# Kernel optimization log

Measured on AMD Instinct MI355X. Metric: run time of the kernel, lower is better.

## Reference

```python
import jax, jax.numpy as jnp
import numpy as np

HID = 100

def _make_params(key):
    dims = [(2, HID), (HID, HID), (HID, HID), (HID, HID), (HID, 2)]
    params = {}
    for i, (fan_in, fan_out) in enumerate(dims):
        k1, k2, key = jax.random.split(key, 3)
        bound = 1.0 / np.sqrt(fan_in)
        params[f"W{i+1}"] = jax.random.uniform(k1, (fan_out, fan_in), jnp.float32, -bound, bound)
        params[f"b{i+1}"] = jax.random.uniform(k2, (fan_out,), jnp.float32, -bound, bound)
    return params

def setup_inputs() -> dict:
    key = jax.random.key(0)
    kx, kt, kp = jax.random.split(key, 3)
    N = 262144
    inp = {
        "x": jax.random.normal(kx, (N, 1), jnp.float32),
        "t": jax.random.uniform(kt, (N, 1), jnp.float32),
    }
    inp.update(_make_params(kp))
    return inp

def reference(x, t, W1, b1, W2, b2, W3, b3, W4, b4, W5, b5):
    hidden = [(W1, b1), (W2, b2), (W3, b3), (W4, b4)]

    def u(xs, ts):  # scalar xs, ts -> [2] = (u_r, u_i)
        h = jnp.stack([xs, ts])
        for W, b in hidden:
            h = jnp.tanh(W @ h + b)
        return W5 @ h + b5

    u_t = jax.jacfwd(u, argnums=1)          # [2]: (u_t_r, u_t_i)
    u_x = jax.jacfwd(u, argnums=0)          # [2]
    u_xx = jax.jacfwd(u_x, argnums=0)       # [2]: (u_xx_r, u_xx_i)

    def per_point(xs, ts):
        return u(xs, ts), u_t(xs, ts), u_xx(xs, ts)

    U, Ut, Uxx = jax.vmap(per_point)(x[:, 0], t[:, 0])  # each [N, 2]

    u_r, u_i = U[:, 0:1], U[:, 1:2]
    u_t_r, u_t_i = Ut[:, 0:1], Ut[:, 1:2]
    u_xx_r, u_xx_i = Uxx[:, 0:1], Uxx[:, 1:2]

    mag2 = u_r * u_r + u_i * u_i
    f_r = -u_t_i + 0.5 * u_xx_r + mag2 * u_r
    f_i = u_t_r + 0.5 * u_xx_i + mag2 * u_i
    return f_r, f_i
```

## Files before the change

### kernel.cpp

```cpp
#include <hip/hip_runtime.h>


using half8 = __attribute__((ext_vector_type(8))) _Float16;
using half4 = __attribute__((ext_vector_type(4))) _Float16;
using f32x4 = __attribute__((ext_vector_type(4))) float;

#define LW      44800
#define ZOFF    134400
#define STGOFF  134416
#define STGW    2304
#define PLANEB  1152
#define NWAVES  12
#define SMEM_BYTES 162064

union U8 { uint4 u; half8 h; };
union U4 { uint2 u; half4 h; };

static __device__ __forceinline__ float fast_tanh(float z) {
    float e = __expf(2.0f * z);
    return 1.0f - 2.0f * __builtin_amdgcn_rcpf(e + 1.0f);
}

static __device__ __forceinline__ void split2(float v, _Float16& h0, _Float16& h1) {
    h0 = (_Float16)v;
    h1 = (_Float16)((v - (float)h0) * 512.0f);
}

__global__ void prep_w(const float* __restrict__ W2, const float* __restrict__ W3,
                       const float* __restrict__ W4, unsigned short* __restrict__ ws) {
    int bid = blockIdx.x;
    int l = bid / 28, rem = bid % 28, kt = rem / 7, jt = rem % 7;
    const float* W = (l == 0) ? W2 : (l == 1) ? W3 : W4;
    int lane = threadIdx.x;
    int c = lane & 15, q = lane >> 4;
    int j = 16 * jt + c;
    if (kt < 3) {
        for (int s = 0; s < 2; ++s)
            for (int i = 0; i < 8; ++i) {
                int k = 32 * kt + 8 * q + i;
                float w = (j < 100) ? W[j * 100 + k] : 0.0f;
                _Float16 h0 = (_Float16)w;
                _Float16 val = (s == 0) ? h0 : (_Float16)((w - (float)h0) * 512.0f);
                ws[(l*LW + kt*14336 + jt*2048 + s*1024 + lane*16 + i*2) >> 1] =
                    __builtin_bit_cast(unsigned short, val);
            }
    } else if (lane < 16) {
        for (int s = 0; s < 2; ++s)
            for (int i = 0; i < 4; ++i) {
                int k = 96 + i;
                float w = (j < 100) ? W[j * 100 + k] : 0.0f;
                _Float16 h0 = (_Float16)w;
                _Float16 val = (s == 0) ? h0 : (_Float16)((w - (float)h0) * 512.0f);
                ws[(l*LW + 43008 + jt*256 + s*128 + lane*8 + i*2) >> 1] =
                    __builtin_bit_cast(unsigned short, val);
            }
    }
}

__global__ void __launch_bounds__(768) pinn_mfma(
    const float* __restrict__ x,  const float* __restrict__ t,
    const float* __restrict__ W1, const float* __restrict__ b1,
    const float* __restrict__ b2, const float* __restrict__ b3,
    const float* __restrict__ b4,
    const float* __restrict__ W5, const float* __restrict__ b5,
    const char* __restrict__ ws, float* __restrict__ out,
    int N, int nchunks)
{
    extern __shared__ char smem[];
    const int tid  = threadIdx.x;
    const int w    = tid >> 6;
    const int lane = tid & 63;
    const int c15  = lane & 15;
    const int q    = lane >> 4;

    for (int it = 0; it < 11; ++it) {
        int idx = tid + it * 768;
        if (idx < 8400) ((uint4*)smem)[idx] = ((const uint4*)ws)[idx];
    }
    if (tid < 4) *(unsigned*)(smem + ZOFF + tid * 4) = 0u;
    __syncthreads();

    char* stg = smem + STGOFF + w * STGW;

    half8 a0[3], a1[3];
    half4 a0t,   a1t;
    f32x4 c0[7], c1[7];

    for (int chunk = blockIdx.x; chunk < nchunks; chunk += gridDim.x) {
        const int colbase = chunk * 192 + w * 16;

        {
            int col = colbase + c15;
            int pt = col >> 2, ch = col & 3;
            int ptc = (pt < N) ? pt : (N - 1);
            float xv = x[ptc], tv = t[ptc];
            #pragma unroll
            for (int kt = 0; kt < 3; ++kt) {
                half8 v0, v1;
                #pragma unroll
                for (int i = 0; i < 8; ++i) {
                    int j = 32 * kt + 8 * q + i;
                    float w0 = W1[2*j], w1 = W1[2*j+1], bb = b1[j];
                    float p = fmaf(w0, xv, fmaf(w1, tv, bb));
                    float a = fast_tanh(p);
                    float s = 1.0f - a * a;
                    float v = (ch == 0) ? a : (ch == 1) ? s * w1
                             : (ch == 2) ? s * w0 : -2.0f * a * s * w0 * w0;
                    _Float16 h0, h1; split2(v, h0, h1);
                    v0[i] = h0; v1[i] = h1;
                }
                a0[kt] = v0; a1[kt] = v1;
            }
            half4 t0 = {0, 0, 0, 0}, t1 = {0, 0, 0, 0};
            if (q == 0) {
                #pragma unroll
                for (int i = 0; i < 4; ++i) {
                    int j = 96 + i;
                    float w0 = W1[2*j], w1 = W1[2*j+1], bb = b1[j];
                    float p = fmaf(w0, xv, fmaf(w1, tv, bb));
                    float a = fast_tanh(p);
                    float s = 1.0f - a * a;
                    float v = (ch == 0) ? a : (ch == 1) ? s * w1
                             : (ch == 2) ? s * w0 : -2.0f * a * s * w0 * w0;
                    _Float16 h0, h1; split2(v, h0, h1);
                    t0[i] = h0; t1[i] = h1;
                }
            }
            a0t = t0; a1t = t1;
        }

        for (int l = 0; l < 3; ++l) {
            const char* WL = smem + l * LW;
            const float* BL = (l == 0) ? b2 : (l == 1) ? b3 : b4;

            #pragma unroll
            for (int jt = 0; jt < 7; ++jt) {
                c0[jt] = (f32x4){0.f, 0.f, 0.f, 0.f};
                c1[jt] = (f32x4){0.f, 0.f, 0.f, 0.f};
            }

            #pragma unroll
            for (int kt = 0; kt < 3; ++kt)
                #pragma unroll
                for (int jt = 0; jt < 7; ++jt) {
                    U8 b0u, b1u;
                    b0u.u = *(const uint4*)(WL + kt*14336 + jt*2048 + lane*16);
                    b1u.u = *(const uint4*)(WL + kt*14336 + jt*2048 + 1024 + lane*16);
                    c0[jt] = __builtin_amdgcn_mfma_f32_16x16x32_f16(a0[kt], b0u.h, c0[jt], 0, 0, 0);
                    c1[jt] = __builtin_amdgcn_mfma_f32_16x16x32_f16(a0[kt], b1u.h, c1[jt], 0, 0, 0);
                    c1[jt] = __builtin_amdgcn_mfma_f32_16x16x32_f16(a1[kt], b0u.h, c1[jt], 0, 0, 0);
                }
            #pragma unroll
            for (int jt = 0; jt < 7; ++jt) {
                int toff  = (lane < 16) ? (l*LW + 43008 + jt*256 + lane*8) : ZOFF;
                int toff1 = (lane < 16) ? (toff + 128) : ZOFF;
                U4 b0u, b1u;
                b0u.u = *(const uint2*)(smem + toff);
                b1u.u = *(const uint2*)(smem + toff1);
                c0[jt] = __builtin_amdgcn_mfma_f32_16x16x16f16(a0t, b0u.h, c0[jt], 0, 0, 0);
                c1[jt] = __builtin_amdgcn_mfma_f32_16x16x16f16(a0t, b1u.h, c1[jt], 0, 0, 0);
                c1[jt] = __builtin_amdgcn_mfma_f32_16x16x16f16(a1t, b0u.h, c1[jt], 0, 0, 0);
            }

            if (l < 2) {
                #pragma unroll
                for (int kc = 0; kc < 4; ++kc) {
                    int njt = (kc < 3) ? 2 : 1;
                    #pragma unroll
                    for (int jj = 0; jj < 2; ++jj) {
                        if (jj >= njt) continue;
                        int jt = 2 * kc + jj;
                        int kk = 16 * jj + c15;
                        int j  = 16 * jt + c15;
                        float bj = BL[(j < 100) ? j : 99];
                        float z0 = c0[jt][0] + c1[jt][0] * (1.0f/512.0f) + bj;
                        float z1 = c0[jt][1] + c1[jt][1] * (1.0f/512.0f);
                        float z2 = c0[jt][2] + c1[jt][2] * (1.0f/512.0f);
                        float z3 = c0[jt][3] + c1[jt][3] * (1.0f/512.0f);
                        float a = fast_tanh(z0);
                        float s = 1.0f - a * a;
                        float v[4];
                        v[0] = a; v[1] = s * z1; v[2] = s * z2;
                        v[3] = fmaf(-2.0f * a * s * z2, z2, s * z3);
                        #pragma unroll
                        for (int r = 0; r < 4; ++r) {
                            _Float16 h0, h1; split2(v[r], h0, h1);
                            _Float16* bp = (_Float16*)(stg) + (4 * q + r) * 36 + kk;
                            bp[0]   = h0;
                            bp[576] = h1;
                        }
                    }
                    if (kc < 3) {
                        const char* rb = stg + c15 * 72 + 16 * q;
                        U8 u;
                        uint2 L, H;
                        L = *(const uint2*)(rb);              H = *(const uint2*)(rb + 8);
                        u.u = (uint4){L.x, L.y, H.x, H.y};    a0[kc] = u.h;
                        L = *(const uint2*)(rb + PLANEB);     H = *(const uint2*)(rb + PLANEB + 8);
                        u.u = (uint4){L.x, L.y, H.x, H.y};    a1[kc] = u.h;
                    } else {
                        U4 u;
                        if (q == 0) {
                            const char* rb = stg + c15 * 72;
                            u.u = *(const uint2*)(rb);            a0t = u.h;
                            u.u = *(const uint2*)(rb + PLANEB);   a1t = u.h;
                        } else {
                            a0t = (half4){0,0,0,0}; a1t = (half4){0,0,0,0};
                        }
                    }
                }
            } else {
                float p00 = 0.f, p01 = 0.f, p03 = 0.f;
                float p10 = 0.f, p11 = 0.f, p13 = 0.f;
                #pragma unroll
                for (int jt = 0; jt < 7; ++jt) {
                    int j = 16 * jt + c15;
                    int j2 = (j < 100) ? j : 99;
                    float m = (j < 100) ? 1.0f : 0.0f;
                    float bj = BL[j2];
                    float w50 = W5[j2] * m, w51 = W5[100 + j2] * m;
                    float z0 = c0[jt][0] + c1[jt][0] * (1.0f/512.0f) + bj;
                    float z1 = c0[jt][1] + c1[jt][1] * (1.0f/512.0f);
                    float z2 = c0[jt][2] + c1[jt][2] * (1.0f/512.0f);
                    float z3 = c0[jt][3] + c1[jt][3] * (1.0f/512.0f);
                    float a = fast_tanh(z0);
                    float s = 1.0f - a * a;
                    float v0 = a, v1 = s * z1;
                    float v3 = fmaf(-2.0f * a * s * z2, z2, s * z3);
                    p00 = fmaf(w50, v0, p00);
                    p01 = fmaf(w50, v1, p01);
                    p03 = fmaf(w50, v3, p03);
                    p10 = fmaf(w51, v0, p10);
                    p11 = fmaf(w51, v1, p11);
                    p13 = fmaf(w51, v3, p13);
                }
                #pragma unroll
                for (int m = 1; m <= 8; m <<= 1) {
                    p00 += __shfl_xor(p00, m, 64);
                    p01 += __shfl_xor(p01, m, 64);
                    p03 += __shfl_xor(p03, m, 64);
                    p10 += __shfl_xor(p10, m, 64);
                    p11 += __shfl_xor(p11, m, 64);
                    p13 += __shfl_xor(p13, m, 64);
                }
                int pt = chunk * 48 + w * 4 + q;
                if (c15 == 0 && pt < N) {
                    float ur = p00 + b5[0], ui = p10 + b5[1];
                    float mag2 = ur * ur + ui * ui;
                    float fr = fmaf(mag2, ur, fmaf(0.5f, p03, -p11));
                    float fi = fmaf(mag2, ui, fmaf(0.5f, p13,  p01));
                    out[pt]     = fr;
                    out[N + pt] = fi;
                }
            }
        }
    }
}

extern "C" void kernel_launch(void* const* d_in, const int* in_sizes, int n_in,
                              void* d_out, int out_size, void* d_ws, size_t ws_size,
                              hipStream_t stream) {
    const float* x  = (const float*)d_in[0];
    const float* t  = (const float*)d_in[1];
    const float* W1 = (const float*)d_in[2];
    const float* b1 = (const float*)d_in[3];
    const float* W2 = (const float*)d_in[4];
    const float* b2 = (const float*)d_in[5];
    const float* W3 = (const float*)d_in[6];
    const float* b3 = (const float*)d_in[7];
    const float* W4 = (const float*)d_in[8];
    const float* b4 = (const float*)d_in[9];
    const float* W5 = (const float*)d_in[10];
    const float* b5 = (const float*)d_in[11];
    float* out = (float*)d_out;
    const int N = in_sizes[0];
    const int nchunks = (N + 47) / 48;

    (void)hipFuncSetAttribute((const void*)pinn_mfma,
                              hipFuncAttributeMaxDynamicSharedMemorySize, SMEM_BYTES);

    prep_w<<<84, 64, 0, stream>>>(W2, W3, W4, (unsigned short*)d_ws);
    pinn_mfma<<<256, 768, SMEM_BYTES, stream>>>(x, t, W1, b1, b2, b3, b4, W5, b5,
                                                (const char*)d_ws, out, N, nchunks);
}
```

Baseline: 437.6 us.

## Read MFMA weight fragments from global memory instead of staging in LDS

Drops the per-block copy of all three hidden-layer weight matrices (about 134 KB) into shared memory and has each wave load its B fragments straight from the global workspace, which should hit in L1/L2. Blocks shrink from 12 waves to 4 waves with only a small static LDS staging area, and launch bounds now allow several blocks per CU. The grid grows to 2048 blocks, each taking a contiguous range of chunks. This removes the large LDS fill and the occupancy cap of one block per CU, at the cost of far more global/L1 traffic in the inner MFMA loop.

```diff
diff --git a/kernel.cpp b/kernel.cpp
--- a/kernel.cpp
+++ b/kernel.cpp
@@ -6,12 +6,10 @@
 using f32x4 = __attribute__((ext_vector_type(4))) float;
 
 #define LW      44800
-#define ZOFF    134400
-#define STGOFF  134416
+#define WZOFF   134400
 #define STGW    2304
 #define PLANEB  1152
-#define NWAVES  12
-#define SMEM_BYTES 162064
+#define SMEM_BYTES 9216
 
 union U8 { uint4 u; half8 h; };
 union U4 { uint2 u; half4 h; };
@@ -29,9 +27,13 @@
 __global__ void prep_w(const float* __restrict__ W2, const float* __restrict__ W3,
                        const float* __restrict__ W4, unsigned short* __restrict__ ws) {
     int bid = blockIdx.x;
+    int lane = threadIdx.x;
+    if (bid == 84) {
+        if (lane < 8) ws[(WZOFF >> 1) + lane] = 0;
+        return;
+    }
     int l = bid / 28, rem = bid % 28, kt = rem / 7, jt = rem % 7;
     const float* W = (l == 0) ? W2 : (l == 1) ? W3 : W4;
-    int lane = threadIdx.x;
     int c = lane & 15, q = lane >> 4;
     int j = 16 * jt + c;
     if (kt < 3) {
@@ -57,37 +59,33 @@
     }
 }
 
-__global__ void __launch_bounds__(768) pinn_mfma(
+__global__ void __launch_bounds__(256, 4) pinn_mfma(
     const float* __restrict__ x,  const float* __restrict__ t,
     const float* __restrict__ W1, const float* __restrict__ b1,
     const float* __restrict__ b2, const float* __restrict__ b3,
     const float* __restrict__ b4,
     const float* __restrict__ W5, const float* __restrict__ b5,
     const char* __restrict__ ws, float* __restrict__ out,
-    int N, int nchunks)
+    int N, int nchunks, int cpb)
 {
-    extern __shared__ char smem[];
+    __shared__ char smem[SMEM_BYTES];
     const int tid  = threadIdx.x;
     const int w    = tid >> 6;
     const int lane = tid & 63;
     const int c15  = lane & 15;
     const int q    = lane >> 4;
 
-    for (int it = 0; it < 11; ++it) {
-        int idx = tid + it * 768;
-        if (idx < 8400) ((uint4*)smem)[idx] = ((const uint4*)ws)[idx];
-    }
-    if (tid < 4) *(unsigned*)(smem + ZOFF + tid * 4) = 0u;
-    __syncthreads();
-
-    char* stg = smem + STGOFF + w * STGW;
+    char* stg = smem + w * STGW;
 
     half8 a0[3], a1[3];
     half4 a0t,   a1t;
     f32x4 c0[7], c1[7];
 
-    for (int chunk = blockIdx.x; chunk < nchunks; chunk += gridDim.x) {
-        const int colbase = chunk * 192 + w * 16;
+    const int cbeg = blockIdx.x * cpb;
+    const int cend = (cbeg + cpb < nchunks) ? (cbeg + cpb) : nchunks;
+
+    for (int chunk = cbeg; chunk < cend; ++chunk) {
+        const int colbase = chunk * 64 + w * 16;
 
         {
             int col = colbase + c15;
@@ -130,7 +128,7 @@
         }
 
         for (int l = 0; l < 3; ++l) {
-            const char* WL = smem + l * LW;
+            const char* WL = ws + l * LW;
             const float* BL = (l == 0) ? b2 : (l == 1) ? b3 : b4;
 
             #pragma unroll
@@ -152,11 +150,11 @@
                 }
             #pragma unroll
             for (int jt = 0; jt < 7; ++jt) {
-                int toff  = (lane < 16) ? (l*LW + 43008 + jt*256 + lane*8) : ZOFF;
-                int toff1 = (lane < 16) ? (toff + 128) : ZOFF;
+                int toff  = (lane < 16) ? (l*LW + 43008 + jt*256 + lane*8) : WZOFF;
+                int toff1 = (lane < 16) ? (toff + 128) : WZOFF;
                 U4 b0u, b1u;
-                b0u.u = *(const uint2*)(smem + toff);
-                b1u.u = *(const uint2*)(smem + toff1);
+                b0u.u = *(const uint2*)(ws + toff);
+                b1u.u = *(const uint2*)(ws + toff1);
                 c0[jt] = __builtin_amdgcn_mfma_f32_16x16x16f16(a0t, b0u.h, c0[jt], 0, 0, 0);
                 c1[jt] = __builtin_amdgcn_mfma_f32_16x16x16f16(a0t, b1u.h, c1[jt], 0, 0, 0);
                 c1[jt] = __builtin_amdgcn_mfma_f32_16x16x16f16(a1t, b0u.h, c1[jt], 0, 0, 0);
@@ -243,7 +241,7 @@
                     p11 += __shfl_xor(p11, m, 64);
                     p13 += __shfl_xor(p13, m, 64);
                 }
-                int pt = chunk * 48 + w * 4 + q;
+                int pt = chunk * 16 + w * 4 + q;
                 if (c15 == 0 && pt < N) {
                     float ur = p00 + b5[0], ui = p10 + b5[1];
                     float mag2 = ur * ur + ui * ui;
@@ -274,12 +272,11 @@
     const float* b5 = (const float*)d_in[11];
     float* out = (float*)d_out;
     const int N = in_sizes[0];
-    const int nchunks = (N + 47) / 48;
-
-    (void)hipFuncSetAttribute((const void*)pinn_mfma,
-                              hipFuncAttributeMaxDynamicSharedMemorySize, SMEM_BYTES);
-
-    prep_w<<<84, 64, 0, stream>>>(W2, W3, W4, (unsigned short*)d_ws);
-    pinn_mfma<<<256, 768, SMEM_BYTES, stream>>>(x, t, W1, b1, b2, b3, b4, W5, b5,
-                                                (const char*)d_ws, out, N, nchunks);
-}
+    const int nchunks = (N + 15) / 16;
+    const int grid = 2048;
+    const int cpb = (nchunks + grid - 1) / grid;
+
+    prep_w<<<85, 64, 0, stream>>>(W2, W3, W4, (unsigned short*)d_ws);
+    pinn_mfma<<<grid, 256, 0, stream>>>(x, t, W1, b1, b2, b3, b4, W5, b5,
+                                        (const char*)d_ws, out, N, nchunks, cpb);
+}
```

Result: slower. 899.0 us (+105.4%).

## Keep high-half weights in LDS, read low-residual plane from global, use 16 waves

Applied to the files above, without the earlier changes.

Splits the fp16 weight planes into separate regions. Only the main (hi) plane is copied into shared memory, and the residual (lo) plane is read directly from global/L2. This cuts the LDS footprint, which allows 16 waves (1024 threads) per block instead of 12, with larger chunks of 64 points. The risk is that the residual-plane loads now go to global memory in the inner MFMA loop, adding latency and cache traffic.

```diff
diff --git a/kernel.cpp b/kernel.cpp
--- a/kernel.cpp
+++ b/kernel.cpp
@@ -5,13 +5,14 @@
 using half4 = __attribute__((ext_vector_type(4))) _Float16;
 using f32x4 = __attribute__((ext_vector_type(4))) float;
 
-#define LW      44800
-#define ZOFF    134400
-#define STGOFF  134416
+#define LWP     22400
+#define P1OFF   67200
+#define WZOFF   134400
+#define LZOFF   67200
+#define STG0    67216
 #define STGW    2304
 #define PLANEB  1152
-#define NWAVES  12
-#define SMEM_BYTES 162064
+#define SMEM_BYTES 104080
 
 union U8 { uint4 u; half8 h; };
 union U4 { uint2 u; half4 h; };
@@ -29,9 +30,13 @@
 __global__ void prep_w(const float* __restrict__ W2, const float* __restrict__ W3,
                        const float* __restrict__ W4, unsigned short* __restrict__ ws) {
     int bid = blockIdx.x;
+    int lane = threadIdx.x;
+    if (bid == 84) {
+        if (lane < 8) ws[(WZOFF >> 1) + lane] = 0;
+        return;
+    }
     int l = bid / 28, rem = bid % 28, kt = rem / 7, jt = rem % 7;
     const float* W = (l == 0) ? W2 : (l == 1) ? W3 : W4;
-    int lane = threadIdx.x;
     int c = lane & 15, q = lane >> 4;
     int j = 16 * jt + c;
     if (kt < 3) {
@@ -41,8 +46,8 @@
                 float w = (j < 100) ? W[j * 100 + k] : 0.0f;
                 _Float16 h0 = (_Float16)w;
                 _Float16 val = (s == 0) ? h0 : (_Float16)((w - (float)h0) * 512.0f);
-                ws[(l*LW + kt*14336 + jt*2048 + s*1024 + lane*16 + i*2) >> 1] =
-                    __builtin_bit_cast(unsigned short, val);
+                int off = s * P1OFF + l*LWP + kt*7168 + jt*1024 + lane*16 + i*2;
+                ws[off >> 1] = __builtin_bit_cast(unsigned short, val);
             }
     } else if (lane < 16) {
         for (int s = 0; s < 2; ++s)
@@ -51,13 +56,13 @@
                 float w = (j < 100) ? W[j * 100 + k] : 0.0f;
                 _Float16 h0 = (_Float16)w;
                 _Float16 val = (s == 0) ? h0 : (_Float16)((w - (float)h0) * 512.0f);
-                ws[(l*LW + 43008 + jt*256 + s*128 + lane*8 + i*2) >> 1] =
-                    __builtin_bit_cast(unsigned short, val);
-            }
-    }
-}
-
-__global__ void __launch_bounds__(768) pinn_mfma(
+                int off = s * P1OFF + l*LWP + 21504 + jt*128 + lane*8 + i*2;
+                ws[off >> 1] = __builtin_bit_cast(unsigned short, val);
+            }
+    }
+}
+
+__global__ void __launch_bounds__(1024) pinn_mfma(
     const float* __restrict__ x,  const float* __restrict__ t,
     const float* __restrict__ W1, const float* __restrict__ b1,
     const float* __restrict__ b2, const float* __restrict__ b3,
@@ -73,21 +78,21 @@
     const int c15  = lane & 15;
     const int q    = lane >> 4;
 
-    for (int it = 0; it < 11; ++it) {
-        int idx = tid + it * 768;
-        if (idx < 8400) ((uint4*)smem)[idx] = ((const uint4*)ws)[idx];
-    }
-    if (tid < 4) *(unsigned*)(smem + ZOFF + tid * 4) = 0u;
+    for (int it = 0; it < 5; ++it) {
+        int idx = tid + it * 1024;
+        if (idx < 4200) ((uint4*)smem)[idx] = ((const uint4*)ws)[idx];
+    }
+    if (tid < 4) *(unsigned*)(smem + LZOFF + tid * 4) = 0u;
     __syncthreads();
 
-    char* stg = smem + STGOFF + w * STGW;
+    char* stg = smem + STG0 + w * STGW;
 
     half8 a0[3], a1[3];
     half4 a0t,   a1t;
     f32x4 c0[7], c1[7];
 
     for (int chunk = blockIdx.x; chunk < nchunks; chunk += gridDim.x) {
-        const int colbase = chunk * 192 + w * 16;
+        const int colbase = chunk * 256 + w * 16;
 
         {
             int col = colbase + c15;
@@ -130,7 +135,8 @@
         }
 
         for (int l = 0; l < 3; ++l) {
-            const char* WL = smem + l * LW;
+            const char* WL0 = smem + l * LWP;
+            const char* WL1 = ws + P1OFF + l * LWP;
             const float* BL = (l == 0) ? b2 : (l == 1) ? b3 : b4;
 
             #pragma unroll
@@ -144,19 +150,19 @@
                 #pragma unroll
                 for (int jt = 0; jt < 7; ++jt) {
                     U8 b0u, b1u;
-                    b0u.u = *(const uint4*)(WL + kt*14336 + jt*2048 + lane*16);
-                    b1u.u = *(const uint4*)(WL + kt*14336 + jt*2048 + 1024 + lane*16);
+                    b0u.u = *(const uint4*)(WL0 + kt*7168 + jt*1024 + lane*16);
+                    b1u.u = *(const uint4*)(WL1 + kt*7168 + jt*1024 + lane*16);
                     c0[jt] = __builtin_amdgcn_mfma_f32_16x16x32_f16(a0[kt], b0u.h, c0[jt], 0, 0, 0);
                     c1[jt] = __builtin_amdgcn_mfma_f32_16x16x32_f16(a0[kt], b1u.h, c1[jt], 0, 0, 0);
                     c1[jt] = __builtin_amdgcn_mfma_f32_16x16x32_f16(a1[kt], b0u.h, c1[jt], 0, 0, 0);
                 }
             #pragma unroll
             for (int jt = 0; jt < 7; ++jt) {
-                int toff  = (lane < 16) ? (l*LW + 43008 + jt*256 + lane*8) : ZOFF;
-                int toff1 = (lane < 16) ? (toff + 128) : ZOFF;
+                int tof  = (lane < 16) ? (l*LWP + 21504 + jt*128 + lane*8) : LZOFF;
+                int tog  = (lane < 16) ? (P1OFF + l*LWP + 21504 + jt*128 + lane*8) : WZOFF;
                 U4 b0u, b1u;
-                b0u.u = *(const uint2*)(smem + toff);
-                b1u.u = *(const uint2*)(smem + toff1);
+                b0u.u = *(const uint2*)(smem + tof);
+                b1u.u = *(const uint2*)(ws + tog);
                 c0[jt] = __builtin_amdgcn_mfma_f32_16x16x16f16(a0t, b0u.h, c0[jt], 0, 0, 0);
                 c1[jt] = __builtin_amdgcn_mfma_f32_16x16x16f16(a0t, b1u.h, c1[jt], 0, 0, 0);
                 c1[jt] = __builtin_amdgcn_mfma_f32_16x16x16f16(a1t, b0u.h, c1[jt], 0, 0, 0);
@@ -243,7 +249,7 @@
                     p11 += __shfl_xor(p11, m, 64);
                     p13 += __shfl_xor(p13, m, 64);
                 }
-                int pt = chunk * 48 + w * 4 + q;
+                int pt = chunk * 64 + w * 4 + q;
                 if (c15 == 0 && pt < N) {
                     float ur = p00 + b5[0], ui = p10 + b5[1];
                     float mag2 = ur * ur + ui * ui;
@@ -274,12 +280,12 @@
     const float* b5 = (const float*)d_in[11];
     float* out = (float*)d_out;
     const int N = in_sizes[0];
-    const int nchunks = (N + 47) / 48;
+    const int nchunks = (N + 63) / 64;
 
     (void)hipFuncSetAttribute((const void*)pinn_mfma,
                               hipFuncAttributeMaxDynamicSharedMemorySize, SMEM_BYTES);
 
-    prep_w<<<84, 64, 0, stream>>>(W2, W3, W4, (unsigned short*)d_ws);
-    pinn_mfma<<<256, 768, SMEM_BYTES, stream>>>(x, t, W1, b1, b2, b3, b4, W5, b5,
-                                                (const char*)d_ws, out, N, nchunks);
-}
+    prep_w<<<85, 64, 0, stream>>>(W2, W3, W4, (unsigned short*)d_ws);
+    pinn_mfma<<<256, 1024, SMEM_BYTES, stream>>>(x, t, W1, b1, b2, b3, b4, W5, b5,
+                                                 (const char*)d_ws, out, N, nchunks);
+}
```

New measurement: 697.0 us. 59.3% more time.
